# Optimization experiments

Hardware: AMD Instinct MI355X
Metric: run time of the kernel (lower is better)

The kernel has to match this reference:

```python
import jax, jax.numpy as jnp
import numpy as np

EMBED_DIM = 128
NUM_HEADS = 16
HEAD_DIM = EMBED_DIM // NUM_HEADS
SCALE = HEAD_DIM ** -0.5


def setup_inputs() -> dict:
    key = jax.random.key(0)
    ks = jax.random.split(key, 9)
    B, S, E = 4, 2048, EMBED_DIM
    s = 1.0 / np.sqrt(E)
    return {
        "x": jax.random.normal(ks[0], (B, S, E), dtype=jnp.float32),
        "Wq": jax.random.uniform(ks[1], (E, E), jnp.float32, -s, s),
        "bq": jax.random.uniform(ks[2], (E,), jnp.float32, -s, s),
        "Wk": jax.random.uniform(ks[3], (E, E), jnp.float32, -s, s),
        "bk": jax.random.uniform(ks[4], (E,), jnp.float32, -s, s),
        "Wv": jax.random.uniform(ks[5], (E, E), jnp.float32, -s, s),
        "bv": jax.random.uniform(ks[6], (E,), jnp.float32, -s, s),
        "Wo": jax.random.uniform(ks[7], (E, E), jnp.float32, -s, s),
        "bo": jax.random.uniform(ks[8], (E,), jnp.float32, -s, s),
    }


def reference(x, Wq, bq, Wk, bk, Wv, bv, Wo, bo):
    B, S, E = x.shape
    H, D = NUM_HEADS, HEAD_DIM
    # projections (torch Linear: x @ W.T + b)
    q = (x @ Wq.T + bq).reshape(B, S, H, D).transpose(0, 2, 1, 3)  # [B,H,S,D]
    k = (x @ Wk.T + bk).reshape(B, S, H, D).transpose(0, 2, 1, 3)
    v = (x @ Wv.T + bv).reshape(B, S, H, D).transpose(0, 2, 1, 3)
    scores = jnp.einsum("bhqd,bhkd->bhqk", q, k) * SCALE  # [B,H,S,S]
    causal_mask = jnp.triu(jnp.ones((S, S), dtype=bool), k=1)  # True above diag
    scores = jnp.where(causal_mask, jnp.float32(-1e9), scores)
    w = jax.nn.sigmoid(scores)
    w = w / jnp.sum(w, axis=-1, keepdims=True)  # sigmoid-sum normalization
    attn = jnp.einsum("bhqk,bhkd->bhqd", w, v)  # [B,H,S,D]
    attn = attn.transpose(0, 2, 1, 3).reshape(B, S, E)
    return attn @ Wo.T + bo
```

## Files before the change

kernel.cpp:

```cpp
#include <hip/hip_runtime.h>
#include <math.h>

#define EDIM 128
#define NHEAD 16
#define HDIM 8
#define SEQ 2048
#define BATCH 4
#define NROW (BATCH*SEQ)
#define QNEG (-0.35355339059327373f * 1.4426950408889634f)

#if __has_builtin(__builtin_amdgcn_exp2f)
#define EXP2F(x) __builtin_amdgcn_exp2f(x)
#else
#define EXP2F(x) exp2f(x)
#endif
#define RCPF(x) __builtin_amdgcn_rcpf(x)

typedef __attribute__((ext_vector_type(8))) short short8v;
typedef __attribute__((ext_vector_type(4))) short short4v;
typedef __attribute__((ext_vector_type(4))) float float4v;

union U16x8 { uint4 u; short8v s; };
union U16x4 { uint2 u; short4v s; };

#if __has_builtin(__builtin_amdgcn_mfma_f32_16x16x16bf16_1k)
#define MFMA_PV(a,b,c) __builtin_amdgcn_mfma_f32_16x16x16bf16_1k(a,b,c,0,0,0)
#else
static __device__ __forceinline__ float4v mfma_pv_asm(short4v a, short4v b, float4v c) {
  float4v d;
  asm("v_mfma_f32_16x16x16_bf16 %0, %1, %2, %3" : "=v"(d) : "v"(a), "v"(b), "v"(c));
  return d;
}
#define MFMA_PV(a,b,c) mfma_pv_asm(a,b,c)
#endif

__device__ __forceinline__ unsigned pk_bf16(float a, float b) {
  unsigned ua = __float_as_uint(a), ub = __float_as_uint(b);
  unsigned lo = (ua + 0x7fffu + ((ua >> 16) & 1u)) >> 16;
  unsigned hi = (ub + 0x7fffu + ((ub >> 16) & 1u)) & 0xffff0000u;
  return lo | hi;
}

__global__ __launch_bounds__(256)
void cast4_kernel(const float* __restrict__ W0, const float* __restrict__ W1,
                  const float* __restrict__ W2, const float* __restrict__ W3,
                  unsigned short* __restrict__ Wb)
{
  const float* W = (blockIdx.y == 0) ? W0 : (blockIdx.y == 1) ? W1
                 : (blockIdx.y == 2) ? W2 : W3;
  unsigned short* o = Wb + (size_t)blockIdx.y * (EDIM * EDIM);
  const int i = (blockIdx.x * 256 + threadIdx.x) * 4;
  const float4 f = *(const float4*)(W + i);
  uint2 p;
  p.x = pk_bf16(f.x, f.y);
  p.y = pk_bf16(f.z, f.w);
  *(uint2*)(o + i) = p;
}

template<int MODE>
__device__ __forceinline__
void proj_mfma(const float* __restrict__ X, const unsigned short* __restrict__ Wb,
               const float* __restrict__ bias, void* __restrict__ out)
{
  __shared__ unsigned short xs[16 * EDIM];
  const int tid = threadIdx.x;
  const int row0 = blockIdx.x * 16;

  {
    const int r = tid >> 4, c16 = tid & 15;
    const float4* src = (const float4*)(X + (size_t)(row0 + r) * EDIM + c16 * 8);
    const float4 f0 = src[0], f1 = src[1];
    uint4 v;
    v.x = pk_bf16(f0.x, f0.y); v.y = pk_bf16(f0.z, f0.w);
    v.z = pk_bf16(f1.x, f1.y); v.w = pk_bf16(f1.z, f1.w);
    const unsigned addr = (unsigned)(r * 256 + c16 * 16) ^ (unsigned)((r & 7) << 4);
    *(uint4*)((char*)xs + addr) = v;
  }
  __syncthreads();

  const int lane = tid & 63, wv = tid >> 6;
  const int lq = lane & 15, qd = lane >> 4;
  const int n0 = wv * 32;

  short8v a[4];
  #pragma unroll
  for (int kk = 0; kk < 4; ++kk) {
    const unsigned addr =
        (unsigned)(lq * 256 + kk * 64 + qd * 16) ^ (unsigned)((lq & 7) << 4);
    a[kk] = *(const short8v*)((const char*)xs + addr);
  }

  float4v D0 = {0.f, 0.f, 0.f, 0.f}, D1 = {0.f, 0.f, 0.f, 0.f};
  const unsigned short* wr0 = Wb + (size_t)(n0 + lq) * EDIM + qd * 8;
  #pragma unroll
  for (int kk = 0; kk < 4; ++kk) {
    U16x8 b0, b1;
    b0.u = *(const uint4*)(wr0 + kk * 32);
    b1.u = *(const uint4*)(wr0 + 16 * EDIM + kk * 32);
    D0 = __builtin_amdgcn_mfma_f32_16x16x32_bf16(a[kk], b0.s, D0, 0, 0, 0);
    D1 = __builtin_amdgcn_mfma_f32_16x16x32_bf16(a[kk], b1.s, D1, 0, 0, 0);
  }

  const int nA = n0 + lq, nB = nA + 16;
  const float bzA = bias[nA], bzB = bias[nB];

  if (MODE == 3) {
    float* of = (float*)out + (size_t)(row0 + qd * 4) * EDIM + nA;
    #pragma unroll
    for (int r = 0; r < 4; ++r) {
      of[r * EDIM]      = D0[r] + bzA;
      of[r * EDIM + 16] = D1[r] + bzB;
    }
    return;
  }

  if (MODE == 2) {
    const int b_ = row0 >> 11, srel = row0 & (SEQ - 1);
    const int tg = srel >> 4;
    unsigned short* oU = (unsigned short*)out;
    {
      const int bh = b_ * NHEAD + (nA >> 3), dv = nA & 7;
      uint2 p;
      p.x = pk_bf16(D0[0] + bzA, D0[1] + bzA);
      p.y = pk_bf16(D0[2] + bzA, D0[3] + bzA);
      *(uint2*)(oU + (size_t)bh * (SEQ * HDIM) + tg * 128 + dv * 16 + qd * 4) = p;
    }
    {
      const int bh = b_ * NHEAD + (nB >> 3), dv = nB & 7;
      uint2 p;
      p.x = pk_bf16(D1[0] + bzB, D1[1] + bzB);
      p.y = pk_bf16(D1[2] + bzB, D1[3] + bzB);
      *(uint2*)(oU + (size_t)bh * (SEQ * HDIM) + tg * 128 + dv * 16 + qd * 4) = p;
    }
    return;
  }

  {
    const int b_ = row0 >> 11;
    const int srel = (row0 & (SEQ - 1)) + qd * 4;
    unsigned short* oU = (unsigned short*)out;
    const int bhA = b_ * NHEAD + (nA >> 3), dvA = nA & 7;
    const int bhB = bhA + 2;
    unsigned short* pA = oU + ((size_t)bhA * SEQ + srel) * 8 + dvA;
    unsigned short* pB = oU + ((size_t)bhB * SEQ + srel) * 8 + dvA;
    #pragma unroll
    for (int r = 0; r < 4; ++r) {
      float vA = D0[r] + bzA, vB = D1[r] + bzB;
      if (MODE == 0) { vA *= QNEG; vB *= QNEG; }
      pA[r * 8] = (unsigned short)pk_bf16(vA, 0.f);
      pB[r * 8] = (unsigned short)pk_bf16(vB, 0.f);
    }
    return;
  }
}

__global__ __launch_bounds__(256)
void qkv_kernel(const float* __restrict__ X, const unsigned short* __restrict__ Wb,
                const float* __restrict__ bq, const float* __restrict__ bk,
                const float* __restrict__ bv,
                unsigned* __restrict__ qb, unsigned* __restrict__ kb,
                unsigned* __restrict__ vb)
{
  const int m = blockIdx.y;
  const unsigned short* wb = Wb + (size_t)m * EDIM * EDIM;
  if (m == 0)      proj_mfma<0>(X, wb, bq, (void*)qb);
  else if (m == 1) proj_mfma<1>(X, wb, bk, (void*)kb);
  else             proj_mfma<2>(X, wb, bv, (void*)vb);
}

__global__ __launch_bounds__(256)
void oproj_kernel(const float* __restrict__ A, const unsigned short* __restrict__ Wbo,
                  const float* __restrict__ bo, float* __restrict__ out)
{
  proj_mfma<3>(A, Wbo, bo, (void*)out);
}

template<bool DIAG>
__device__ __forceinline__
float4v attn_step(short8v kf, short8v qf, short4v vf, float4v acc,
                  int laneq, int quad)
{
  const float4v z = {0.f, 0.f, 0.f, 0.f};
  float4v st = __builtin_amdgcn_mfma_f32_16x16x32_bf16(kf, qf, z, 0, 0, 0);
  unsigned rb[4];
  #pragma unroll
  for (int r = 0; r < 4; ++r) {
    float s = RCPF(1.f + EXP2F(st[r]));
    if (DIAG) s = (4 * quad + r <= laneq) ? s : 0.f;
    rb[r] = __float_as_uint(s) + 0x8000u;
  }
  U16x4 p;
  p.u.x = __builtin_amdgcn_perm(rb[1], rb[0], 0x07060302u);
  p.u.y = __builtin_amdgcn_perm(rb[3], rb[2], 0x07060302u);
  return MFMA_PV(p.s, vf, acc);
}

__device__ __forceinline__
short4v load_vfrag(const unsigned short* __restrict__ Vtbh, int t,
                   int quad, int d, bool is8)
{
  const unsigned short* p = Vtbh + t * 128 + d * 16 + 4 * quad;
  const uint2 v = *(const uint2*)p;
  U16x4 vf;
  vf.u.x = is8 ? 0x3F803F80u : v.x;
  vf.u.y = is8 ? 0x3F803F80u : v.y;
  return vf.s;
}

__device__ __forceinline__
void epilogue(float4v acc, int T, int bh, int laneq, int quad,
              float* __restrict__ out)
{
  const int b_ = bh >> 4, h = bh & 15;
  const int pidx = (quad * 16 + 8) << 2;
  #pragma unroll
  for (int r = 0; r < 4; ++r) {
    const float den = __int_as_float(
        __builtin_amdgcn_ds_bpermute(pidx, __float_as_int(acc[r])));
    const float val = acc[r] * RCPF(den);
    const int row = 16 * T + 4 * quad + r;
    if (laneq < 8)
      out[(size_t)(b_ * SEQ + row) * EDIM + h * HDIM + laneq] = val;
  }
}

__global__ __launch_bounds__(128, 8)
void attn_kernel(const unsigned* __restrict__ Qb, const unsigned* __restrict__ Kb,
                 const unsigned* __restrict__ Vb, float* __restrict__ out)
{
  __shared__ float cmb[2][64][4];

  const int bh    = blockIdx.x & 63;
  const int g     = blockIdx.x >> 6;
  const int w     = threadIdx.x >> 6;
  const int lane  = threadIdx.x & 63;
  const int laneq = lane & 15;
  const int quad  = lane >> 4;
  const int L = g, H = 127 - g;
  const int mL = (L + 1) >> 1, mH = (H + 1) >> 1;
  const int d   = laneq & 7;
  const bool is8 = (laneq == 8);

  const uint4* Kg = (const uint4*)Kb + (size_t)bh * 2048;
  const uint4* Qg = (const uint4*)Qb + (size_t)bh * 2048;
  const unsigned short* Vtbh = (const unsigned short*)Vb + (size_t)bh * SEQ * HDIM;

  U16x8 qfl, qfh;
  {
    const uint4 rl = Qg[16 * L + laneq];
    const uint4 rh = Qg[16 * H + laneq];
    qfl.u = (lane < 16) ? rl : make_uint4(0u, 0u, 0u, 0u);
    qfh.u = (lane < 16) ? rh : make_uint4(0u, 0u, 0u, 0u);
  }

  float4v accL = {0.f, 0.f, 0.f, 0.f};
  float4v accH = {0.f, 0.f, 0.f, 0.f};

  if (w == 0) {
    U16x8 kf; kf.u = Kg[laneq];
    short4v vf = load_vfrag(Vtbh, 0, quad, d, is8);
    #pragma unroll 2
    for (int t = 0; t < mH; ++t) {
      U16x8 kn; kn.u = Kg[16 * (t + 1) + laneq];
      short4v vn = load_vfrag(Vtbh, t + 1, quad, d, is8);
      if (t < mL) accL = attn_step<false>(kf.s, qfl.s, vf, accL, laneq, quad);
      accH = attn_step<false>(kf.s, qfh.s, vf, accH, laneq, quad);
      kf = kn; vf = vn;
    }
  } else {
    U16x8 kf; kf.u = Kg[16 * mL + laneq];
    short4v vf = load_vfrag(Vtbh, mL, quad, d, is8);
    #pragma unroll 2
    for (int t = mL; t < L; ++t) {
      U16x8 kn; kn.u = Kg[16 * (t + 1) + laneq];
      short4v vn = load_vfrag(Vtbh, t + 1, quad, d, is8);
      accL = attn_step<false>(kf.s, qfl.s, vf, accL, laneq, quad);
      kf = kn; vf = vn;
    }
    accL = attn_step<true>(kf.s, qfl.s, vf, accL, laneq, quad);
    kf.u = Kg[16 * mH + laneq];
    vf = load_vfrag(Vtbh, mH, quad, d, is8);
    #pragma unroll 2
    for (int t = mH; t < H; ++t) {
      U16x8 kn; kn.u = Kg[16 * (t + 1) + laneq];
      short4v vn = load_vfrag(Vtbh, t + 1, quad, d, is8);
      accH = attn_step<false>(kf.s, qfh.s, vf, accH, laneq, quad);
      kf = kn; vf = vn;
    }
    accH = attn_step<true>(kf.s, qfh.s, vf, accH, laneq, quad);

    *(float4*)&cmb[0][lane][0] = make_float4(accL[0], accL[1], accL[2], accL[3]);
    *(float4*)&cmb[1][lane][0] = make_float4(accH[0], accH[1], accH[2], accH[3]);
  }
  __syncthreads();

  if (w == 0) {
    const float4 pL = *(const float4*)&cmb[0][lane][0];
    const float4 pH = *(const float4*)&cmb[1][lane][0];
    accL[0] += pL.x; accL[1] += pL.y; accL[2] += pL.z; accL[3] += pL.w;
    accH[0] += pH.x; accH[1] += pH.y; accH[2] += pH.z; accH[3] += pH.w;
    epilogue(accL, L, bh, laneq, quad, out);
    epilogue(accH, H, bh, laneq, quad, out);
  }
}

extern "C" void kernel_launch(void* const* d_in, const int* in_sizes, int n_in,
                              void* d_out, int out_size, void* d_ws, size_t ws_size,
                              hipStream_t stream)
{
  const float* x  = (const float*)d_in[0];
  const float* Wq = (const float*)d_in[1];
  const float* bq = (const float*)d_in[2];
  const float* Wk = (const float*)d_in[3];
  const float* bk = (const float*)d_in[4];
  const float* Wv = (const float*)d_in[5];
  const float* bv = (const float*)d_in[6];
  const float* Wo = (const float*)d_in[7];
  const float* bo = (const float*)d_in[8];

  float* ws = (float*)d_ws;
  unsigned short* Wb = (unsigned short*)ws;
  float*    attn = ws + 65536;
  unsigned* Qb   = (unsigned*)(ws + 65536 + 1048576);
  unsigned* Kb   = Qb + (size_t)524288;
  unsigned* Vb   = Kb + (size_t)524288;

  cast4_kernel<<<dim3(16, 4), 256, 0, stream>>>(Wq, Wk, Wv, Wo, Wb);
  qkv_kernel<<<dim3(NROW / 16, 3), 256, 0, stream>>>(x, Wb, bq, bk, bv, Qb, Kb, Vb);
  attn_kernel<<<dim3(4096), 128, 0, stream>>>(Qb, Kb, Vb, attn);
  oproj_kernel<<<dim3(NROW / 16), 256, 0, stream>>>(attn, Wb + 3 * EDIM * EDIM, bo,
                                                    (float*)d_out);
}
```

Before: 122.0 us.

## Drop weight cast kernel and fuse Q/K/V projections into one pass

Removes the separate weight-to-bf16 cast launch; each projection block now reads fp32 weights directly and converts them to bf16 in registers before the MFMA. The three Q/K/V projections are merged into a single kernel that stages and converts each X tile once, then runs all three weight tiles against the same A fragments. This saves one launch, two extra reads and conversions of X, and the grid dimension over projections. In exchange, every block reads twice as many weight bytes (fp32) and repeats the conversion work, and each block does three times more work serially.

```diff
diff --git a/kernel.cpp b/kernel.cpp
--- a/kernel.cpp
+++ b/kernel.cpp
@@ -41,62 +41,25 @@
   return lo | hi;
 }
 
-__global__ __launch_bounds__(256)
-void cast4_kernel(const float* __restrict__ W0, const float* __restrict__ W1,
-                  const float* __restrict__ W2, const float* __restrict__ W3,
-                  unsigned short* __restrict__ Wb)
-{
-  const float* W = (blockIdx.y == 0) ? W0 : (blockIdx.y == 1) ? W1
-                 : (blockIdx.y == 2) ? W2 : W3;
-  unsigned short* o = Wb + (size_t)blockIdx.y * (EDIM * EDIM);
-  const int i = (blockIdx.x * 256 + threadIdx.x) * 4;
-  const float4 f = *(const float4*)(W + i);
-  uint2 p;
-  p.x = pk_bf16(f.x, f.y);
-  p.y = pk_bf16(f.z, f.w);
-  *(uint2*)(o + i) = p;
-}
-
 template<int MODE>
 __device__ __forceinline__
-void proj_mfma(const float* __restrict__ X, const unsigned short* __restrict__ Wb,
-               const float* __restrict__ bias, void* __restrict__ out)
-{
-  __shared__ unsigned short xs[16 * EDIM];
-  const int tid = threadIdx.x;
-  const int row0 = blockIdx.x * 16;
-
-  {
-    const int r = tid >> 4, c16 = tid & 15;
-    const float4* src = (const float4*)(X + (size_t)(row0 + r) * EDIM + c16 * 8);
-    const float4 f0 = src[0], f1 = src[1];
-    uint4 v;
-    v.x = pk_bf16(f0.x, f0.y); v.y = pk_bf16(f0.z, f0.w);
-    v.z = pk_bf16(f1.x, f1.y); v.w = pk_bf16(f1.z, f1.w);
-    const unsigned addr = (unsigned)(r * 256 + c16 * 16) ^ (unsigned)((r & 7) << 4);
-    *(uint4*)((char*)xs + addr) = v;
-  }
-  __syncthreads();
-
-  const int lane = tid & 63, wv = tid >> 6;
-  const int lq = lane & 15, qd = lane >> 4;
-  const int n0 = wv * 32;
-
-  short8v a[4];
+void run_tile(const short8v a[4], const float* __restrict__ W,
+              const float* __restrict__ bias, void* __restrict__ out,
+              int row0, int lq, int qd, int n0)
+{
+  float4v D0 = {0.f, 0.f, 0.f, 0.f}, D1 = {0.f, 0.f, 0.f, 0.f};
+  const float* wr = W + (size_t)(n0 + lq) * EDIM + qd * 8;
   #pragma unroll
   for (int kk = 0; kk < 4; ++kk) {
-    const unsigned addr =
-        (unsigned)(lq * 256 + kk * 64 + qd * 16) ^ (unsigned)((lq & 7) << 4);
-    a[kk] = *(const short8v*)((const char*)xs + addr);
-  }
-
-  float4v D0 = {0.f, 0.f, 0.f, 0.f}, D1 = {0.f, 0.f, 0.f, 0.f};
-  const unsigned short* wr0 = Wb + (size_t)(n0 + lq) * EDIM + qd * 8;
-  #pragma unroll
-  for (int kk = 0; kk < 4; ++kk) {
+    const float4 f0 = *(const float4*)(wr + kk * 32);
+    const float4 f1 = *(const float4*)(wr + kk * 32 + 4);
+    const float4 g0 = *(const float4*)(wr + 16 * EDIM + kk * 32);
+    const float4 g1 = *(const float4*)(wr + 16 * EDIM + kk * 32 + 4);
     U16x8 b0, b1;
-    b0.u = *(const uint4*)(wr0 + kk * 32);
-    b1.u = *(const uint4*)(wr0 + 16 * EDIM + kk * 32);
+    b0.u = make_uint4(pk_bf16(f0.x, f0.y), pk_bf16(f0.z, f0.w),
+                      pk_bf16(f1.x, f1.y), pk_bf16(f1.z, f1.w));
+    b1.u = make_uint4(pk_bf16(g0.x, g0.y), pk_bf16(g0.z, g0.w),
+                      pk_bf16(g1.x, g1.y), pk_bf16(g1.z, g1.w));
     D0 = __builtin_amdgcn_mfma_f32_16x16x32_bf16(a[kk], b0.s, D0, 0, 0, 0);
     D1 = __builtin_amdgcn_mfma_f32_16x16x32_bf16(a[kk], b1.s, D1, 0, 0, 0);
   }
@@ -154,25 +117,64 @@
   }
 }
 
+__device__ __forceinline__
+void stage_and_afrags(const float* __restrict__ X, unsigned short* xs,
+                      int row0, int tid, short8v a[4])
+{
+  {
+    const int r = tid >> 4, c16 = tid & 15;
+    const float4* src = (const float4*)(X + (size_t)(row0 + r) * EDIM + c16 * 8);
+    const float4 f0 = src[0], f1 = src[1];
+    uint4 v;
+    v.x = pk_bf16(f0.x, f0.y); v.y = pk_bf16(f0.z, f0.w);
+    v.z = pk_bf16(f1.x, f1.y); v.w = pk_bf16(f1.z, f1.w);
+    const unsigned addr = (unsigned)(r * 256 + c16 * 16) ^ (unsigned)((r & 7) << 4);
+    *(uint4*)((char*)xs + addr) = v;
+  }
+  __syncthreads();
+  const int lane = tid & 63;
+  const int lq = lane & 15, qd = lane >> 4;
+  #pragma unroll
+  for (int kk = 0; kk < 4; ++kk) {
+    const unsigned addr =
+        (unsigned)(lq * 256 + kk * 64 + qd * 16) ^ (unsigned)((lq & 7) << 4);
+    a[kk] = *(const short8v*)((const char*)xs + addr);
+  }
+}
+
 __global__ __launch_bounds__(256)
-void qkv_kernel(const float* __restrict__ X, const unsigned short* __restrict__ Wb,
-                const float* __restrict__ bq, const float* __restrict__ bk,
-                const float* __restrict__ bv,
-                unsigned* __restrict__ qb, unsigned* __restrict__ kb,
-                unsigned* __restrict__ vb)
-{
-  const int m = blockIdx.y;
-  const unsigned short* wb = Wb + (size_t)m * EDIM * EDIM;
-  if (m == 0)      proj_mfma<0>(X, wb, bq, (void*)qb);
-  else if (m == 1) proj_mfma<1>(X, wb, bk, (void*)kb);
-  else             proj_mfma<2>(X, wb, bv, (void*)vb);
+void qkv_fused_kernel(const float* __restrict__ X,
+                      const float* __restrict__ Wq, const float* __restrict__ Wk,
+                      const float* __restrict__ Wv,
+                      const float* __restrict__ bq, const float* __restrict__ bk,
+                      const float* __restrict__ bv,
+                      unsigned* __restrict__ qb, unsigned* __restrict__ kb,
+                      unsigned* __restrict__ vb)
+{
+  __shared__ unsigned short xs[16 * EDIM];
+  const int tid = threadIdx.x;
+  const int row0 = blockIdx.x * 16;
+  short8v a[4];
+  stage_and_afrags(X, xs, row0, tid, a);
+  const int lane = tid & 63, wv = tid >> 6;
+  const int lq = lane & 15, qd = lane >> 4, n0 = wv * 32;
+  run_tile<0>(a, Wq, bq, (void*)qb, row0, lq, qd, n0);
+  run_tile<1>(a, Wk, bk, (void*)kb, row0, lq, qd, n0);
+  run_tile<2>(a, Wv, bv, (void*)vb, row0, lq, qd, n0);
 }
 
 __global__ __launch_bounds__(256)
-void oproj_kernel(const float* __restrict__ A, const unsigned short* __restrict__ Wbo,
+void oproj_kernel(const float* __restrict__ A, const float* __restrict__ Wo,
                   const float* __restrict__ bo, float* __restrict__ out)
 {
-  proj_mfma<3>(A, Wbo, bo, (void*)out);
+  __shared__ unsigned short xs[16 * EDIM];
+  const int tid = threadIdx.x;
+  const int row0 = blockIdx.x * 16;
+  short8v a[4];
+  stage_and_afrags(A, xs, row0, tid, a);
+  const int lane = tid & 63, wv = tid >> 6;
+  const int lq = lane & 15, qd = lane >> 4, n0 = wv * 32;
+  run_tile<3>(a, Wo, bo, (void*)out, row0, lq, qd, n0);
 }
 
 template<bool DIAG>
@@ -319,15 +321,13 @@
   const float* bo = (const float*)d_in[8];
 
   float* ws = (float*)d_ws;
-  unsigned short* Wb = (unsigned short*)ws;
   float*    attn = ws + 65536;
   unsigned* Qb   = (unsigned*)(ws + 65536 + 1048576);
   unsigned* Kb   = Qb + (size_t)524288;
   unsigned* Vb   = Kb + (size_t)524288;
 
-  cast4_kernel<<<dim3(16, 4), 256, 0, stream>>>(Wq, Wk, Wv, Wo, Wb);
-  qkv_kernel<<<dim3(NROW / 16, 3), 256, 0, stream>>>(x, Wb, bq, bk, bv, Qb, Kb, Vb);
+  qkv_fused_kernel<<<dim3(NROW / 16), 256, 0, stream>>>(x, Wq, Wk, Wv, bq, bk, bv,
+                                                        Qb, Kb, Vb);
   attn_kernel<<<dim3(4096), 128, 0, stream>>>(Qb, Kb, Vb, attn);
-  oproj_kernel<<<dim3(NROW / 16), 256, 0, stream>>>(attn, Wb + 3 * EDIM * EDIM, bo,
-                                                    (float*)d_out);
-}
+  oproj_kernel<<<dim3(NROW / 16), 256, 0, stream>>>(attn, Wo, bo, (float*)d_out);
+}
```

Measured after the change: 128.3 us. 1.05x slower.
